# Kernel tuning notes

Measured on AMD Instinct MI355X. Metric: run time of the kernel, lower is better.

The kernel has to match this reference:

```python
import jax, jax.numpy as jnp
import numpy as np

C = 256
NUM_HEADS = 4


def setup_inputs() -> dict:
    key = jax.random.key(0)
    ks = jax.random.split(key, 7)
    B, H, W = 4, 64, 64
    s = 1.0 / np.sqrt(C)
    return {
        "x": jax.random.normal(ks[0], (B, C, H, W), dtype=jnp.float32),
        "ln_gamma": jnp.ones((C,), jnp.float32),
        "ln_beta": jnp.zeros((C,), jnp.float32),
        "w_qkv": jax.random.normal(ks[1], (C, 3 * C), dtype=jnp.float32) * s,
        "b_qkv": jnp.zeros((3 * C,), jnp.float32),
        "w_proj": jax.random.normal(ks[2], (C, C), dtype=jnp.float32) * s,
        "b_proj": jnp.zeros((C,), jnp.float32),
    }


def reference(x, ln_gamma, ln_beta, w_qkv, b_qkv, w_proj, b_proj):
    B, Cc, H, W = x.shape
    N = H * W
    hd = Cc // NUM_HEADS
    # [B, N, C] token layout
    x_ = jnp.transpose(x, (0, 2, 3, 1)).reshape(B, N, Cc)
    # LayerNorm over channel dim
    mu = jnp.mean(x_, axis=-1, keepdims=True)
    var = jnp.mean(jnp.square(x_ - mu), axis=-1, keepdims=True)
    xn = (x_ - mu) * jax.lax.rsqrt(var + 1e-5) * ln_gamma + ln_beta
    qkv = xn @ w_qkv + b_qkv  # [B, N, 3C]
    q, k, v = jnp.split(qkv, 3, axis=-1)
    # [B, heads, N, hd]
    q = q.reshape(B, N, NUM_HEADS, hd).transpose(0, 2, 1, 3)
    k = k.reshape(B, N, NUM_HEADS, hd).transpose(0, 2, 1, 3)
    v = v.reshape(B, N, NUM_HEADS, hd).transpose(0, 2, 1, 3)
    # NOTE: source scales by 1/sqrt(C), not 1/sqrt(head_dim)
    scores = jnp.einsum("bhnd,bhmd->bhnm", q, k) / jnp.sqrt(jnp.float32(Cc))
    attn = jax.nn.softmax(scores, axis=-1)
    out = jnp.einsum("bhnm,bhmd->bhnd", attn, v)
    out = out.transpose(0, 2, 1, 3).reshape(B, N, Cc)
    out = out @ w_proj + b_proj
    out = out.reshape(B, H, W, Cc).transpose(0, 3, 1, 2)
    return x + out
```

## Files before the change

kernel.cpp:

```cpp
#include <hip/hip_runtime.h>
#include <hip/hip_bf16.h>

typedef __bf16 bf16_t;
typedef bf16_t bf16x8 __attribute__((ext_vector_type(8)));
typedef bf16_t bf16x4v __attribute__((ext_vector_type(4)));
typedef float f32x4 __attribute__((ext_vector_type(4)));
typedef float f32x16 __attribute__((ext_vector_type(16)));
typedef int i32x4 __attribute__((ext_vector_type(4)));
typedef int i32x2 __attribute__((ext_vector_type(2)));

constexpr int C = 256;
constexpr int Bb = 4;
constexpr int N = 4096;
constexpr int NH = 4;
constexpr int HD = 64;
constexpr float SM_SCALE_LOG2E = 0.0625f * 1.44269504088896340736f;

__device__ __forceinline__ int swz_chunk(int row, int chunk) {
  return row * 128 + ((chunk ^ (row & 7)) << 4);
}

__device__ __forceinline__ f32x4 mfma16(bf16x8 a, bf16x8 b, f32x4 c) {
  return __builtin_amdgcn_mfma_f32_16x16x32_bf16(a, b, c, 0, 0, 0);
}
__device__ __forceinline__ f32x16 mfma32(bf16x8 a, bf16x8 b, f32x16 c) {
  return __builtin_amdgcn_mfma_f32_32x32x16_bf16(a, b, c, 0, 0, 0);
}

__device__ __forceinline__ void glds16(const void* g, void* l) {
  __builtin_amdgcn_global_load_lds(
      (const __attribute__((address_space(1))) void*)g,
      (__attribute__((address_space(3))) void*)l, 16, 0, 0);
}

__device__ __forceinline__ int cvt_pk_bf16(float lo, float hi) {
  int d;
  asm("v_cvt_pk_bf16_f32 %0, %1, %2" : "=v"(d) : "v"(lo), "v"(hi));
  return d;
}
__device__ __forceinline__ i32x2 plswap(int a, int b) {
  return __builtin_amdgcn_permlane32_swap(a, b, false, false);
}
__device__ __forceinline__ float xhalf_max(float v) {
  i32x2 r = plswap(__float_as_int(v), __float_as_int(v));
  return fmaxf(__int_as_float(r[0]), __int_as_float(r[1]));
}
__device__ __forceinline__ float xhalf_sum(float v) {
  i32x2 r = plswap(__float_as_int(v), __float_as_int(v));
  return __int_as_float(r[0]) + __int_as_float(r[1]);
}

__global__ __launch_bounds__(256, 2) void ln_kernel(
    const float* __restrict__ x, const float* __restrict__ gamma,
    const float* __restrict__ beta, bf16_t* __restrict__ xn) {
  __shared__ float tile[256][65];
  __shared__ float red[2][4][64];
  __shared__ float mu_s[64], rs_s[64];
  int tid = threadIdx.x, lane = tid & 63, wv = tid >> 6;
  int b = blockIdx.x >> 6;
  int n0 = (blockIdx.x & 63) << 6;
  const float* xb = x + ((size_t)b * C) * N + n0;
  #pragma unroll 4
  for (int i = 0; i < 64; ++i) {
    int c = wv * 64 + i;
    tile[c][lane] = xb[(size_t)c * N + lane];
  }
  __syncthreads();
  float s = 0.f, s2 = 0.f;
  #pragma unroll 8
  for (int i = 0; i < 64; ++i) {
    float v = tile[wv * 64 + i][lane];
    s += v; s2 += v * v;
  }
  red[0][wv][lane] = s; red[1][wv][lane] = s2;
  __syncthreads();
  if (tid < 64) {
    float ts  = red[0][0][tid] + red[0][1][tid] + red[0][2][tid] + red[0][3][tid];
    float ts2 = red[1][0][tid] + red[1][1][tid] + red[1][2][tid] + red[1][3][tid];
    float mu  = ts * (1.f / 256.f);
    float var = fmaxf(ts2 * (1.f / 256.f) - mu * mu, 0.f);
    mu_s[tid] = mu;
    rs_s[tid] = rsqrtf(var + 1e-5f);
  }
  __syncthreads();
  float g = gamma[tid], be = beta[tid];
  bf16_t* xo = xn + ((size_t)(b * N + n0)) * C + tid;
  #pragma unroll 4
  for (int i = 0; i < 64; ++i) {
    float v = (tile[tid][i] - mu_s[i]) * rs_s[i] * g + be;
    xo[(size_t)i * C] = (bf16_t)v;
  }
}

__global__ void conv_w(const float* __restrict__ wqkv, const float* __restrict__ wproj,
                       bf16_t* __restrict__ wqkvT, bf16_t* __restrict__ wprojT) {
  int id = blockIdx.x * 256 + threadIdx.x;
  if (id < 768 * 256) {
    int nn = id >> 8, kk = id & 255;
    wqkvT[id] = (bf16_t)wqkv[(size_t)kk * 768 + nn];
  }
  if (id < 256 * 256) {
    int nn = id >> 8, kk = id & 255;
    wprojT[id] = (bf16_t)wproj[(size_t)kk * 256 + nn];
  }
}

__global__ __launch_bounds__(256, 2) void gemm_qkv(
    const bf16_t* __restrict__ xn, const bf16_t* __restrict__ wT,
    const float* __restrict__ bias,
    bf16_t* __restrict__ Q, bf16_t* __restrict__ K, bf16_t* __restrict__ Vt) {
  __shared__ char smem[32768];
  char* As = smem;
  char* Bs = smem + 16384;
  int tid = threadIdx.x, lane = tid & 63, wv = tid >> 6;
  int mt = blockIdx.x & 127, nt = blockIdx.x >> 7;
  int m0 = mt * 128, ncol0 = nt * 128;
  int wr = wv >> 1, wc = wv & 1;
  f32x4 acc[4][4];
  #pragma unroll
  for (int i = 0; i < 4; ++i)
    #pragma unroll
    for (int j = 0; j < 4; ++j) acc[i][j] = (f32x4){0.f, 0.f, 0.f, 0.f};
  int q = lane >> 4;
  for (int kt = 0; kt < 4; ++kt) {
    int k0 = kt * 64;
    __syncthreads();
    #pragma unroll
    for (int it = 0; it < 4; ++it) {
      int idx = it * 256 + tid, row = idx >> 3, cb = idx & 7;
      *(i32x4*)(As + swz_chunk(row, cb)) =
          *(const i32x4*)(xn + (size_t)(m0 + row) * C + k0 + cb * 8);
      *(i32x4*)(Bs + swz_chunk(row, cb)) =
          *(const i32x4*)(wT + (size_t)(ncol0 + row) * C + k0 + cb * 8);
    }
    __syncthreads();
    bf16x8 a[4][2];
    #pragma unroll
    for (int mi = 0; mi < 4; ++mi) {
      int ar = wr * 64 + mi * 16 + (lane & 15);
      a[mi][0] = *(const bf16x8*)(As + swz_chunk(ar, q));
      a[mi][1] = *(const bf16x8*)(As + swz_chunk(ar, 4 + q));
    }
    #pragma unroll
    for (int ci = 0; ci < 4; ++ci) {
      int br = wc * 64 + ci * 16 + (lane & 15);
      bf16x8 b0 = *(const bf16x8*)(Bs + swz_chunk(br, q));
      bf16x8 b1 = *(const bf16x8*)(Bs + swz_chunk(br, 4 + q));
      #pragma unroll
      for (int mi = 0; mi < 4; ++mi) {
        acc[mi][ci] = mfma16(a[mi][1], b1, mfma16(a[mi][0], b0, acc[mi][ci]));
      }
    }
  }
  #pragma unroll
  for (int ci = 0; ci < 4; ++ci) {
    int cg = ncol0 + wc * 64 + ci * 16 + (lane & 15);
    float bv = bias[cg];
    int sect = cg >> 8;
    int cc = cg & 255;
    int h = cc >> 6, d = cc & 63;
    #pragma unroll
    for (int mi = 0; mi < 4; ++mi) {
      #pragma unroll
      for (int j = 0; j < 4; ++j) {
        int m = m0 + wr * 64 + mi * 16 + (lane >> 4) * 4 + j;
        int b_ = m >> 12, n = m & 4095;
        float v = acc[mi][ci][j] + bv;
        if (sect == 0) {
          Q[((size_t)((b_ * NH + h) * N + n)) * HD + d] = (bf16_t)(v * SM_SCALE_LOG2E);
        } else if (sect == 1) {
          K[((size_t)((b_ * NH + h) * N + n)) * HD + d] = (bf16_t)v;
        } else {
          Vt[((size_t)((b_ * NH + h) * HD + d)) * N + n] = (bf16_t)v;
        }
      }
    }
  }
}

__global__ __launch_bounds__(512, 4) void attn_kernel(
    const bf16_t* __restrict__ Q, const bf16_t* __restrict__ K,
    const bf16_t* __restrict__ Vt, bf16_t* __restrict__ aout) {
  __shared__ char smem[67584];
  int tid = threadIdx.x, lane = tid & 63, wv = tid >> 6;
  int hi = lane >> 5, qL = lane & 31;
  int wq = wv >> 1, par = wv & 1;
  int bh = blockIdx.x >> 5, qt = blockIdx.x & 31;
  int q0 = qt * 128;

  const bf16_t* Kbh = K + (size_t)bh * N * HD;
  const bf16_t* Vbh = Vt + (size_t)bh * HD * N;
  int sr = tid >> 3;
  int sc = (tid & 7) ^ (sr & 7);

  {
    char* lb = smem;
    glds16(Kbh + (size_t)sr * HD + sc * 8,            lb + tid * 16);
    glds16(Vbh + (size_t)sr * N + sc * 8,             lb + 8192 + tid * 16);
    glds16(Kbh + (size_t)(64 + sr) * HD + sc * 8,     lb + 16384 + tid * 16);
    glds16(Vbh + (size_t)sr * N + 64 + sc * 8,        lb + 24576 + tid * 16);
  }
  char* Qt = smem + 32768;
  const bf16_t* Qbase = Q + ((size_t)bh * N + q0) * HD;
  #pragma unroll
  for (int it = 0; it < 2; ++it) {
    int idx = it * 512 + tid;
    int row = idx >> 3, cb = idx & 7;
    *(i32x4*)(Qt + swz_chunk(row, cb)) =
        *(const i32x4*)(Qbase + (size_t)row * HD + cb * 8);
  }
  __syncthreads();
  bf16x8 qb[4];
  #pragma unroll
  for (int hs = 0; hs < 4; ++hs)
    qb[hs] = *(const bf16x8*)(Qt + swz_chunk(wq * 32 + qL, hs * 2 + hi));

  float m_r = -3.0e38f, l_r = 0.f;
  f32x16 o0, o1;
  #pragma unroll
  for (int i = 0; i < 16; ++i) { o0[i] = 0.f; o1[i] = 0.f; }

  for (int adv = 0; adv < 32; ++adv) {
    __syncthreads();
    if (adv < 31) {
      int n1 = (adv + 1) * 128;
      char* lb = smem + (((adv + 1) & 1) << 15);
      glds16(Kbh + (size_t)(n1 + sr) * HD + sc * 8,        lb + tid * 16);
      glds16(Vbh + (size_t)sr * N + n1 + sc * 8,           lb + 8192 + tid * 16);
      glds16(Kbh + (size_t)(n1 + 64 + sr) * HD + sc * 8,   lb + 16384 + tid * 16);
      glds16(Vbh + (size_t)sr * N + n1 + 64 + sc * 8,      lb + 24576 + tid * 16);
    }
    char* kbase = smem + ((adv & 1) << 15) + par * 16384;
    char* vbase = kbase + 8192;
    f32x16 s0, s1;
    #pragma unroll
    for (int i = 0; i < 16; ++i) { s0[i] = 0.f; s1[i] = 0.f; }
    #pragma unroll
    for (int hs = 0; hs < 4; ++hs) {
      bf16x8 ka0 = *(const bf16x8*)(kbase + swz_chunk(qL, hs * 2 + hi));
      bf16x8 ka1 = *(const bf16x8*)(kbase + swz_chunk(32 + qL, hs * 2 + hi));
      s0 = mfma32(ka0, qb[hs], s0);
      s1 = mfma32(ka1, qb[hs], s1);
    }
    float q0m = fmaxf(fmaxf(s0[0], s0[1]), fmaxf(s0[2], s0[3]));
    float q1m = fmaxf(fmaxf(s0[4], s0[5]), fmaxf(s0[6], s0[7]));
    float q2m = fmaxf(fmaxf(s0[8], s0[9]), fmaxf(s0[10], s0[11]));
    float q3m = fmaxf(fmaxf(s0[12], s0[13]), fmaxf(s0[14], s0[15]));
    float q4m = fmaxf(fmaxf(s1[0], s1[1]), fmaxf(s1[2], s1[3]));
    float q5m = fmaxf(fmaxf(s1[4], s1[5]), fmaxf(s1[6], s1[7]));
    float q6m = fmaxf(fmaxf(s1[8], s1[9]), fmaxf(s1[10], s1[11]));
    float q7m = fmaxf(fmaxf(s1[12], s1[13]), fmaxf(s1[14], s1[15]));
    float tm = fmaxf(fmaxf(fmaxf(q0m, q1m), fmaxf(q2m, q3m)),
                     fmaxf(fmaxf(q4m, q5m), fmaxf(q6m, q7m)));
    tm = xhalf_max(tm);
    if (!__all(tm - m_r <= 8.f)) {
      float nm = fmaxf(m_r, tm);
      float f = __builtin_amdgcn_exp2f(m_r - nm);
      l_r *= f;
      o0 *= f; o1 *= f;
      m_r = nm;
    }
    float rs = 0.f;
    #pragma unroll
    for (int i = 0; i < 16; ++i) {
      float p = __builtin_amdgcn_exp2f(s0[i] - m_r); s0[i] = p; rs += p;
    }
    #pragma unroll
    for (int i = 0; i < 16; ++i) {
      float p = __builtin_amdgcn_exp2f(s1[i] - m_r); s1[i] = p; rs += p;
    }
    l_r += xhalf_sum(rs);
    #pragma unroll
    for (int t16 = 0; t16 < 4; ++t16) {
      int dE0, dE1, dO0, dO1;
      if (t16 < 2) {
        dE0 = cvt_pk_bf16(s0[t16 * 8 + 0], s0[t16 * 8 + 1]);
        dE1 = cvt_pk_bf16(s0[t16 * 8 + 2], s0[t16 * 8 + 3]);
        dO0 = cvt_pk_bf16(s0[t16 * 8 + 4], s0[t16 * 8 + 5]);
        dO1 = cvt_pk_bf16(s0[t16 * 8 + 6], s0[t16 * 8 + 7]);
      } else {
        dE0 = cvt_pk_bf16(s1[(t16 - 2) * 8 + 0], s1[(t16 - 2) * 8 + 1]);
        dE1 = cvt_pk_bf16(s1[(t16 - 2) * 8 + 2], s1[(t16 - 2) * 8 + 3]);
        dO0 = cvt_pk_bf16(s1[(t16 - 2) * 8 + 4], s1[(t16 - 2) * 8 + 5]);
        dO1 = cvt_pk_bf16(s1[(t16 - 2) * 8 + 6], s1[(t16 - 2) * 8 + 7]);
      }
      i32x2 rA = plswap(dE0, dO0);
      i32x2 rB = plswap(dE1, dO1);
      union { i32x4 i; bf16x8 h; } u;
      u.i = (i32x4){rA[0], rB[0], rA[1], rB[1]};
      bf16x8 va0 = *(const bf16x8*)(vbase + swz_chunk(qL, t16 * 2 + hi));
      bf16x8 va1 = *(const bf16x8*)(vbase + swz_chunk(32 + qL, t16 * 2 + hi));
      o0 = mfma32(va0, u.h, o0);
      o1 = mfma32(va1, u.h, o1);
    }
  }

  __syncthreads();
  float* mlb = (float*)(smem + 65536);
  if (hi == 0) {
    mlb[(wv * 32 + qL) * 2]     = m_r;
    mlb[(wv * 32 + qL) * 2 + 1] = l_r;
  }
  __syncthreads();
  float m_p = mlb[((wv ^ 1) * 32 + qL) * 2];
  float l_p = mlb[((wv ^ 1) * 32 + qL) * 2 + 1];
  float M = fmaxf(m_r, m_p);
  float w_s = __builtin_amdgcn_exp2f(m_r - M);
  float l_tot = l_r * w_s + l_p * __builtin_amdgcn_exp2f(m_p - M);
  char* obuf = smem + wq * 8192;
  if (par == 0) {
    #pragma unroll
    for (int g = 0; g < 8; ++g) {
      f32x4 t;
      #pragma unroll
      for (int j = 0; j < 4; ++j)
        t[j] = (g < 4 ? o0[g * 4 + j] : o1[(g - 4) * 4 + j]) * w_s;
      *(f32x4*)(obuf + swz_chunk(lane, g)) = t;
    }
  }
  __syncthreads();
  if (par == 1) {
    float inv = 1.f / l_tot;
    int qglob = q0 + wq * 32 + qL;
    int b_ = bh >> 2, h = bh & 3;
    bf16_t* ab = aout + ((size_t)b_ * N + qglob) * C + h * HD;
    #pragma unroll
    for (int g = 0; g < 8; ++g) {
      f32x4 part = *(const f32x4*)(obuf + swz_chunk(lane, g));
      int hdb = g >> 2, gg = g & 3;
      bf16x4v ov;
      #pragma unroll
      for (int j = 0; j < 4; ++j) {
        float own = hdb ? o1[gg * 4 + j] : o0[gg * 4 + j];
        ov[j] = (bf16_t)((part[j] + own * w_s) * inv);
      }
      *(bf16x4v*)(ab + hdb * 32 + gg * 8 + hi * 4) = ov;
    }
  }
}

__global__ __launch_bounds__(256, 4) void gemm_proj(
    const bf16_t* __restrict__ aout, const bf16_t* __restrict__ wT,
    const float* __restrict__ bias, const float* __restrict__ x,
    float* __restrict__ out) {
  __shared__ char smem[2 * 8192];
  char* As = smem;
  char* Bs = smem + 8192;
  int tid = threadIdx.x, lane = tid & 63, wv = tid >> 6;
  int mt = blockIdx.x & 255, nt = blockIdx.x >> 8;
  int m0 = mt * 64, c0 = nt * 64;
  f32x4 acc[4];
  #pragma unroll
  for (int i = 0; i < 4; ++i) acc[i] = (f32x4){0.f, 0.f, 0.f, 0.f};
  for (int kt = 0; kt < 4; ++kt) {
    int k0 = kt * 64;
    __syncthreads();
    #pragma unroll
    for (int it = 0; it < 2; ++it) {
      int idx = it * 256 + tid, row = idx >> 3, cb = idx & 7;
      *(i32x4*)(As + swz_chunk(row, cb)) =
          *(const i32x4*)(aout + (size_t)(m0 + row) * C + k0 + cb * 8);
      *(i32x4*)(Bs + swz_chunk(row, cb)) =
          *(const i32x4*)(wT + (size_t)(c0 + row) * C + k0 + cb * 8);
    }
    __syncthreads();
    int r = wv * 16 + (lane & 15), q = lane >> 4;
    bf16x8 a0 = *(const bf16x8*)(As + swz_chunk(r, q));
    bf16x8 a1 = *(const bf16x8*)(As + swz_chunk(r, 4 + q));
    #pragma unroll
    for (int ct = 0; ct < 4; ++ct) {
      int br = ct * 16 + (lane & 15);
      bf16x8 b0 = *(const bf16x8*)(Bs + swz_chunk(br, q));
      bf16x8 b1 = *(const bf16x8*)(Bs + swz_chunk(br, 4 + q));
      acc[ct] = mfma16(a0, b0, acc[ct]);
      acc[ct] = mfma16(a1, b1, acc[ct]);
    }
  }
  #pragma unroll
  for (int ct = 0; ct < 4; ++ct) {
    int c = c0 + ct * 16 + (lane & 15);
    float bv = bias[c];
    int m = m0 + wv * 16 + (lane >> 4) * 4;
    int b_ = m >> 12, n = m & 4095;
    size_t off = ((size_t)(b_ * C + c)) * N + n;
    f32x4 xin = *(const f32x4*)(x + off);
    f32x4 res;
    #pragma unroll
    for (int j = 0; j < 4; ++j) res[j] = xin[j] + acc[ct][j] + bv;
    *(f32x4*)(out + off) = res;
  }
}

extern "C" void kernel_launch(void* const* d_in, const int* in_sizes, int n_in,
                              void* d_out, int out_size, void* d_ws, size_t ws_size,
                              hipStream_t stream) {
  const float* x     = (const float*)d_in[0];
  const float* gam   = (const float*)d_in[1];
  const float* bet   = (const float*)d_in[2];
  const float* wqkv  = (const float*)d_in[3];
  const float* bqkv  = (const float*)d_in[4];
  const float* wproj = (const float*)d_in[5];
  const float* bproj = (const float*)d_in[6];
  float* out = (float*)d_out;

  char* ws = (char*)d_ws;
  size_t off = 0;
  auto alloc = [&](size_t bytes) {
    void* p = ws + off;
    off += (bytes + 255) & ~(size_t)255;
    return p;
  };
  bf16_t* xn     = (bf16_t*)alloc((size_t)Bb * N * C * 2);
  bf16_t* wqkvT  = (bf16_t*)alloc((size_t)768 * 256 * 2);
  bf16_t* wprojT = (bf16_t*)alloc((size_t)256 * 256 * 2);
  bf16_t* Qb     = (bf16_t*)alloc((size_t)Bb * NH * N * HD * 2);
  bf16_t* Kb     = (bf16_t*)alloc((size_t)Bb * NH * N * HD * 2);
  bf16_t* Vtb    = (bf16_t*)alloc((size_t)Bb * NH * HD * N * 2);
  bf16_t* aout   = (bf16_t*)alloc((size_t)Bb * N * C * 2);
  if (ws_size < off) return;

  hipLaunchKernelGGL(ln_kernel, dim3(Bb * 64), dim3(256), 0, stream, x, gam, bet, xn);
  hipLaunchKernelGGL(conv_w, dim3(768), dim3(256), 0, stream, wqkv, wproj, wqkvT, wprojT);
  hipLaunchKernelGGL(gemm_qkv, dim3(128 * 6), dim3(256), 0, stream, xn, wqkvT, bqkv,
                     Qb, Kb, Vtb);
  hipLaunchKernelGGL(attn_kernel, dim3(16 * 32), dim3(512), 0, stream,
                     Qb, Kb, Vtb, aout);
  hipLaunchKernelGGL(gemm_proj, dim3(256 * 4), dim3(256), 0, stream, aout, wprojT,
                     bproj, x, out);
}
```

Before: 198.7 us.

## Retile LN, weight transpose and projection GEMM; compute softmax denominator via MFMA

LayerNorm now works on 32-token tiles with twice as many blocks and writes vectorized 4-channel bf16 stores. The weight-conversion kernel transposes through a shared-memory tile so both reads and writes are coalesced. Attention drops the per-iteration VALU row-sum and cross-half swap, accumulating the softmax denominator with an extra MFMA against a ones vector, and uses a flatter max reduction. The projection GEMM moves to 128x128 tiles with a 4x4 accumulator per wave for more operand reuse, at the cost of fewer blocks (256) and higher register pressure.

```diff
diff --git a/kernel.cpp b/kernel.cpp
--- a/kernel.cpp
+++ b/kernel.cpp
@@ -45,63 +45,77 @@
   i32x2 r = plswap(__float_as_int(v), __float_as_int(v));
   return fmaxf(__int_as_float(r[0]), __int_as_float(r[1]));
 }
-__device__ __forceinline__ float xhalf_sum(float v) {
-  i32x2 r = plswap(__float_as_int(v), __float_as_int(v));
-  return __int_as_float(r[0]) + __int_as_float(r[1]);
-}
-
-__global__ __launch_bounds__(256, 2) void ln_kernel(
+
+__global__ __launch_bounds__(256, 4) void ln_kernel(
     const float* __restrict__ x, const float* __restrict__ gamma,
     const float* __restrict__ beta, bf16_t* __restrict__ xn) {
-  __shared__ float tile[256][65];
-  __shared__ float red[2][4][64];
-  __shared__ float mu_s[64], rs_s[64];
-  int tid = threadIdx.x, lane = tid & 63, wv = tid >> 6;
-  int b = blockIdx.x >> 6;
-  int n0 = (blockIdx.x & 63) << 6;
-  const float* xb = x + ((size_t)b * C) * N + n0;
-  #pragma unroll 4
-  for (int i = 0; i < 64; ++i) {
-    int c = wv * 64 + i;
-    tile[c][lane] = xb[(size_t)c * N + lane];
+  __shared__ float tile[256][33];
+  __shared__ float red[2][8][32];
+  __shared__ float mu_s[32], rs_s[32];
+  int tid = threadIdx.x;
+  int b = blockIdx.x >> 7;
+  int n0 = (blockIdx.x & 127) << 5;
+  const float* xb = x + (size_t)b * C * N + n0;
+  int tok = tid & 31, cg = tid >> 5;
+  #pragma unroll 8
+  for (int i = 0; i < 32; ++i) {
+    int c = cg * 32 + i;
+    tile[c][tok] = xb[(size_t)c * N + tok];
   }
   __syncthreads();
   float s = 0.f, s2 = 0.f;
   #pragma unroll 8
-  for (int i = 0; i < 64; ++i) {
-    float v = tile[wv * 64 + i][lane];
+  for (int i = 0; i < 32; ++i) {
+    float v = tile[cg * 32 + i][tok];
     s += v; s2 += v * v;
   }
-  red[0][wv][lane] = s; red[1][wv][lane] = s2;
-  __syncthreads();
-  if (tid < 64) {
-    float ts  = red[0][0][tid] + red[0][1][tid] + red[0][2][tid] + red[0][3][tid];
-    float ts2 = red[1][0][tid] + red[1][1][tid] + red[1][2][tid] + red[1][3][tid];
+  red[0][cg][tok] = s; red[1][cg][tok] = s2;
+  __syncthreads();
+  if (tid < 32) {
+    float ts = 0.f, ts2 = 0.f;
+    #pragma unroll
+    for (int g = 0; g < 8; ++g) { ts += red[0][g][tid]; ts2 += red[1][g][tid]; }
     float mu  = ts * (1.f / 256.f);
     float var = fmaxf(ts2 * (1.f / 256.f) - mu * mu, 0.f);
     mu_s[tid] = mu;
     rs_s[tid] = rsqrtf(var + 1e-5f);
   }
   __syncthreads();
-  float g = gamma[tid], be = beta[tid];
-  bf16_t* xo = xn + ((size_t)(b * N + n0)) * C + tid;
-  #pragma unroll 4
-  for (int i = 0; i < 64; ++i) {
-    float v = (tile[tid][i] - mu_s[i]) * rs_s[i] * g + be;
-    xo[(size_t)i * C] = (bf16_t)v;
-  }
-}
-
-__global__ void conv_w(const float* __restrict__ wqkv, const float* __restrict__ wproj,
-                       bf16_t* __restrict__ wqkvT, bf16_t* __restrict__ wprojT) {
-  int id = blockIdx.x * 256 + threadIdx.x;
-  if (id < 768 * 256) {
-    int nn = id >> 8, kk = id & 255;
-    wqkvT[id] = (bf16_t)wqkv[(size_t)kk * 768 + nn];
-  }
-  if (id < 256 * 256) {
-    int nn = id >> 8, kk = id & 255;
-    wprojT[id] = (bf16_t)wproj[(size_t)kk * 256 + nn];
+  int ch = (tid & 63) * 4, tg = tid >> 6;
+  f32x4 gm = *(const f32x4*)(gamma + ch);
+  f32x4 bt = *(const f32x4*)(beta + ch);
+  #pragma unroll
+  for (int t = 0; t < 8; ++t) {
+    int to = t * 4 + tg;
+    float mu = mu_s[to], rs = rs_s[to];
+    bf16x4v ov;
+    #pragma unroll
+    for (int j = 0; j < 4; ++j)
+      ov[j] = (bf16_t)((tile[ch + j][to] - mu) * rs * gm[j] + bt[j]);
+    *(bf16x4v*)(xn + ((size_t)(b * N + n0 + to)) * C + ch) = ov;
+  }
+}
+
+__global__ __launch_bounds__(256) void conv_w(
+    const float* __restrict__ wqkv, const float* __restrict__ wproj,
+    bf16_t* __restrict__ wqkvT, bf16_t* __restrict__ wprojT) {
+  __shared__ float t[64][65];
+  int blk = blockIdx.x, tid = threadIdx.x;
+  const float* src; bf16_t* dst; int W, rt, ct;
+  if (blk < 48) { src = wqkv; dst = wqkvT; W = 768; rt = blk / 12; ct = blk % 12; }
+  else { int b2 = blk - 48; src = wproj; dst = wprojT; W = 256; rt = b2 >> 2; ct = b2 & 3; }
+  int r0 = rt * 64, c0 = ct * 64;
+  int cc = tid & 63, r4 = tid >> 6;
+  #pragma unroll
+  for (int i = 0; i < 16; ++i) {
+    int rr = i * 4 + r4;
+    t[rr][cc] = src[(size_t)(r0 + rr) * W + c0 + cc];
+  }
+  __syncthreads();
+  #pragma unroll
+  for (int i = 0; i < 16; ++i) {
+    int nn = i * 4 + r4;
+    dst[(size_t)(c0 + nn) * 256 + r0 + cc] = (bf16_t)t[cc][nn];
   }
 }
 
@@ -215,10 +229,14 @@
   for (int hs = 0; hs < 4; ++hs)
     qb[hs] = *(const bf16x8*)(Qt + swz_chunk(wq * 32 + qL, hs * 2 + hi));
 
-  float m_r = -3.0e38f, l_r = 0.f;
-  f32x16 o0, o1;
-  #pragma unroll
-  for (int i = 0; i < 16; ++i) { o0[i] = 0.f; o1[i] = 0.f; }
+  bf16x8 onesf;
+  #pragma unroll
+  for (int i = 0; i < 8; ++i) onesf[i] = (bf16_t)1.0f;
+
+  float m_r = -3.0e38f;
+  f32x16 o0, o1, lacc;
+  #pragma unroll
+  for (int i = 0; i < 16; ++i) { o0[i] = 0.f; o1[i] = 0.f; lacc[i] = 0.f; }
 
   for (int adv = 0; adv < 32; ++adv) {
     __syncthreads();
@@ -242,34 +260,33 @@
       s0 = mfma32(ka0, qb[hs], s0);
       s1 = mfma32(ka1, qb[hs], s1);
     }
-    float q0m = fmaxf(fmaxf(s0[0], s0[1]), fmaxf(s0[2], s0[3]));
-    float q1m = fmaxf(fmaxf(s0[4], s0[5]), fmaxf(s0[6], s0[7]));
-    float q2m = fmaxf(fmaxf(s0[8], s0[9]), fmaxf(s0[10], s0[11]));
-    float q3m = fmaxf(fmaxf(s0[12], s0[13]), fmaxf(s0[14], s0[15]));
-    float q4m = fmaxf(fmaxf(s1[0], s1[1]), fmaxf(s1[2], s1[3]));
-    float q5m = fmaxf(fmaxf(s1[4], s1[5]), fmaxf(s1[6], s1[7]));
-    float q6m = fmaxf(fmaxf(s1[8], s1[9]), fmaxf(s1[10], s1[11]));
-    float q7m = fmaxf(fmaxf(s1[12], s1[13]), fmaxf(s1[14], s1[15]));
-    float tm = fmaxf(fmaxf(fmaxf(q0m, q1m), fmaxf(q2m, q3m)),
-                     fmaxf(fmaxf(q4m, q5m), fmaxf(q6m, q7m)));
+    float t0 = fmaxf(fmaxf(s0[0], s0[1]), s0[2]);
+    float t1 = fmaxf(fmaxf(s0[3], s0[4]), s0[5]);
+    float t2 = fmaxf(fmaxf(s0[6], s0[7]), s0[8]);
+    float t3 = fmaxf(fmaxf(s0[9], s0[10]), s0[11]);
+    float t4 = fmaxf(fmaxf(s0[12], s0[13]), s0[14]);
+    float t5 = fmaxf(fmaxf(s0[15], s1[0]), s1[1]);
+    float t6 = fmaxf(fmaxf(s1[2], s1[3]), s1[4]);
+    float t7 = fmaxf(fmaxf(s1[5], s1[6]), s1[7]);
+    float t8 = fmaxf(fmaxf(s1[8], s1[9]), s1[10]);
+    float t9 = fmaxf(fmaxf(s1[11], s1[12]), s1[13]);
+    float ta = fmaxf(s1[14], s1[15]);
+    float u0 = fmaxf(fmaxf(t0, t1), t2);
+    float u1 = fmaxf(fmaxf(t3, t4), t5);
+    float u2 = fmaxf(fmaxf(t6, t7), t8);
+    float u3 = fmaxf(t9, ta);
+    float tm = fmaxf(fmaxf(u0, u1), fmaxf(u2, u3));
     tm = xhalf_max(tm);
     if (!__all(tm - m_r <= 8.f)) {
       float nm = fmaxf(m_r, tm);
       float f = __builtin_amdgcn_exp2f(m_r - nm);
-      l_r *= f;
-      o0 *= f; o1 *= f;
+      o0 *= f; o1 *= f; lacc *= f;
       m_r = nm;
     }
-    float rs = 0.f;
-    #pragma unroll
-    for (int i = 0; i < 16; ++i) {
-      float p = __builtin_amdgcn_exp2f(s0[i] - m_r); s0[i] = p; rs += p;
-    }
-    #pragma unroll
-    for (int i = 0; i < 16; ++i) {
-      float p = __builtin_amdgcn_exp2f(s1[i] - m_r); s1[i] = p; rs += p;
-    }
-    l_r += xhalf_sum(rs);
+    #pragma unroll
+    for (int i = 0; i < 16; ++i) s0[i] = __builtin_amdgcn_exp2f(s0[i] - m_r);
+    #pragma unroll
+    for (int i = 0; i < 16; ++i) s1[i] = __builtin_amdgcn_exp2f(s1[i] - m_r);
     #pragma unroll
     for (int t16 = 0; t16 < 4; ++t16) {
       int dE0, dE1, dO0, dO1;
@@ -292,8 +309,10 @@
       bf16x8 va1 = *(const bf16x8*)(vbase + swz_chunk(32 + qL, t16 * 2 + hi));
       o0 = mfma32(va0, u.h, o0);
       o1 = mfma32(va1, u.h, o1);
-    }
-  }
+      lacc = mfma32(onesf, u.h, lacc);
+    }
+  }
+  float l_r = lacc[0];
 
   __syncthreads();
   float* mlb = (float*)(smem + 65536);
@@ -339,24 +358,28 @@
   }
 }
 
-__global__ __launch_bounds__(256, 4) void gemm_proj(
+__global__ __launch_bounds__(256, 2) void gemm_proj(
     const bf16_t* __restrict__ aout, const bf16_t* __restrict__ wT,
     const float* __restrict__ bias, const float* __restrict__ x,
     float* __restrict__ out) {
-  __shared__ char smem[2 * 8192];
+  __shared__ char smem[32768];
   char* As = smem;
-  char* Bs = smem + 8192;
+  char* Bs = smem + 16384;
   int tid = threadIdx.x, lane = tid & 63, wv = tid >> 6;
-  int mt = blockIdx.x & 255, nt = blockIdx.x >> 8;
-  int m0 = mt * 64, c0 = nt * 64;
-  f32x4 acc[4];
-  #pragma unroll
-  for (int i = 0; i < 4; ++i) acc[i] = (f32x4){0.f, 0.f, 0.f, 0.f};
+  int mt = blockIdx.x >> 1, nt = blockIdx.x & 1;
+  int m0 = mt * 128, c0 = nt * 128;
+  int wr = wv >> 1, wc = wv & 1;
+  f32x4 acc[4][4];
+  #pragma unroll
+  for (int i = 0; i < 4; ++i)
+    #pragma unroll
+    for (int j = 0; j < 4; ++j) acc[i][j] = (f32x4){0.f, 0.f, 0.f, 0.f};
+  int q = lane >> 4;
   for (int kt = 0; kt < 4; ++kt) {
     int k0 = kt * 64;
     __syncthreads();
     #pragma unroll
-    for (int it = 0; it < 2; ++it) {
+    for (int it = 0; it < 4; ++it) {
       int idx = it * 256 + tid, row = idx >> 3, cb = idx & 7;
       *(i32x4*)(As + swz_chunk(row, cb)) =
           *(const i32x4*)(aout + (size_t)(m0 + row) * C + k0 + cb * 8);
@@ -364,30 +387,39 @@
           *(const i32x4*)(wT + (size_t)(c0 + row) * C + k0 + cb * 8);
     }
     __syncthreads();
-    int r = wv * 16 + (lane & 15), q = lane >> 4;
-    bf16x8 a0 = *(const bf16x8*)(As + swz_chunk(r, q));
-    bf16x8 a1 = *(const bf16x8*)(As + swz_chunk(r, 4 + q));
-    #pragma unroll
-    for (int ct = 0; ct < 4; ++ct) {
-      int br = ct * 16 + (lane & 15);
+    bf16x8 a[4][2];
+    #pragma unroll
+    for (int mi = 0; mi < 4; ++mi) {
+      int ar = wr * 64 + mi * 16 + (lane & 15);
+      a[mi][0] = *(const bf16x8*)(As + swz_chunk(ar, q));
+      a[mi][1] = *(const bf16x8*)(As + swz_chunk(ar, 4 + q));
+    }
+    #pragma unroll
+    for (int ci = 0; ci < 4; ++ci) {
+      int br = wc * 64 + ci * 16 + (lane & 15);
       bf16x8 b0 = *(const bf16x8*)(Bs + swz_chunk(br, q));
       bf16x8 b1 = *(const bf16x8*)(Bs + swz_chunk(br, 4 + q));
-      acc[ct] = mfma16(a0, b0, acc[ct]);
-      acc[ct] = mfma16(a1, b1, acc[ct]);
-    }
-  }
-  #pragma unroll
-  for (int ct = 0; ct < 4; ++ct) {
-    int c = c0 + ct * 16 + (lane & 15);
+      #pragma unroll
+      for (int mi = 0; mi < 4; ++mi) {
+        acc[mi][ci] = mfma16(a[mi][1], b1, mfma16(a[mi][0], b0, acc[mi][ci]));
+      }
+    }
+  }
+  #pragma unroll
+  for (int ci = 0; ci < 4; ++ci) {
+    int c = c0 + wc * 64 + ci * 16 + (lane & 15);
     float bv = bias[c];
-    int m = m0 + wv * 16 + (lane >> 4) * 4;
-    int b_ = m >> 12, n = m & 4095;
-    size_t off = ((size_t)(b_ * C + c)) * N + n;
-    f32x4 xin = *(const f32x4*)(x + off);
-    f32x4 res;
-    #pragma unroll
-    for (int j = 0; j < 4; ++j) res[j] = xin[j] + acc[ct][j] + bv;
-    *(f32x4*)(out + off) = res;
+    #pragma unroll
+    for (int mi = 0; mi < 4; ++mi) {
+      int m = m0 + wr * 64 + mi * 16 + (lane >> 4) * 4;
+      int b_ = m >> 12, n = m & 4095;
+      size_t off = ((size_t)(b_ * C + c)) * N + n;
+      f32x4 xin = *(const f32x4*)(x + off);
+      f32x4 res;
+      #pragma unroll
+      for (int j = 0; j < 4; ++j) res[j] = xin[j] + acc[mi][ci][j] + bv;
+      *(f32x4*)(out + off) = res;
+    }
   }
 }
 
@@ -419,12 +451,12 @@
   bf16_t* aout   = (bf16_t*)alloc((size_t)Bb * N * C * 2);
   if (ws_size < off) return;
 
-  hipLaunchKernelGGL(ln_kernel, dim3(Bb * 64), dim3(256), 0, stream, x, gam, bet, xn);
-  hipLaunchKernelGGL(conv_w, dim3(768), dim3(256), 0, stream, wqkv, wproj, wqkvT, wprojT);
+  hipLaunchKernelGGL(ln_kernel, dim3(Bb * 128), dim3(256), 0, stream, x, gam, bet, xn);
+  hipLaunchKernelGGL(conv_w, dim3(64), dim3(256), 0, stream, wqkv, wproj, wqkvT, wprojT);
   hipLaunchKernelGGL(gemm_qkv, dim3(128 * 6), dim3(256), 0, stream, xn, wqkvT, bqkv,
                      Qb, Kb, Vtb);
   hipLaunchKernelGGL(attn_kernel, dim3(16 * 32), dim3(512), 0, stream,
                      Qb, Kb, Vtb, aout);
-  hipLaunchKernelGGL(gemm_proj, dim3(256 * 4), dim3(256), 0, stream, aout, wprojT,
+  hipLaunchKernelGGL(gemm_proj, dim3(128 * 2), dim3(256), 0, stream, aout, wprojT,
                      bproj, x, out);
 }
```

After: 196.4 us. Within noise of the previous version (-1.2%).
